# Optimization experiments

Hardware: AMD Instinct MI355X
Metric: run time of the kernel (lower is better)

Reference implementation:

```python
import jax, jax.numpy as jnp
import numpy as np

D = 2048          # input_dim == dec_hidden_size
S = 16384         # src_time_steps
H = 250           # projection hidden (hard-coded in module)


def setup_inputs() -> dict:
    key = jax.random.key(0)
    ks = jax.random.split(key, 12)
    sc_d = 1.0 / np.sqrt(D)
    sc_3d = 1.0 / np.sqrt(3 * D)
    sc_h = 1.0 / np.sqrt(H)
    return {
        "s_prev": jax.random.normal(ks[0], (1, 1, D), jnp.float32),
        "enc_hs": jax.random.normal(ks[1], (1, S, D), jnp.float32),
        "cur_men_rep": jax.random.normal(ks[2], (1, 1, D), jnp.float32),
        "src_mask": jax.random.randint(ks[3], (1, S), 0, 2, jnp.int32),
        "W_info": jax.random.normal(ks[4], (D, D), jnp.float32) * sc_d,
        "W_ctx": jax.random.normal(ks[5], (D, D), jnp.float32) * sc_d,
        "W_q": jax.random.normal(ks[6], (D, D), jnp.float32) * sc_d,
        "b_q": jnp.zeros((D,), jnp.float32),
        "W_p1": jax.random.normal(ks[7], (H, 3 * D), jnp.float32) * sc_3d,
        "b_p1": jnp.zeros((H,), jnp.float32),
        "W_p2": jax.random.normal(ks[8], (1, H), jnp.float32) * sc_h,
        "b_p2": jnp.zeros((1,), jnp.float32),
    }


def reference(s_prev, enc_hs, cur_men_rep, src_mask,
              W_info, W_ctx, W_q, b_q, W_p1, b_p1, W_p2, b_p2):
    # dh = linear_info(cur_men_rep): [1,1,D]; uh = linear_ctx(enc_hs): [1,S,D]
    dh = jnp.einsum('bqe,de->bqd', cur_men_rep, W_info)
    uh = jnp.einsum('bse,de->bsd', enc_hs, W_ctx)
    wq = jnp.einsum('bqe,de->bqd', s_prev, W_q) + b_q
    # cat(uh, wq.repeat, dh.repeat) -> tanh : [1,S,3D]
    wquh = jnp.tanh(jnp.concatenate(
        [uh, jnp.broadcast_to(wq, uh.shape), jnp.broadcast_to(dh, uh.shape)],
        axis=2))
    # projection: Linear(3D,250) -> Dropout(eval: identity) -> ReLU -> Linear(250,1)
    h = jax.nn.relu(jnp.einsum('bsk,hk->bsh', wquh, W_p1) + b_p1)
    scores = (jnp.einsum('bsh,oh->bso', h, W_p2) + b_p2).squeeze()   # [S] (B=1)
    scores = jnp.where(src_mask.squeeze().astype(bool), -jnp.inf, scores)
    attn = jax.nn.softmax(scores, axis=-1)                            # [S]
    ctx = jnp.sum(enc_hs * attn[None, :, None], axis=1)               # [1,D]
    return attn, ctx
```

## Files before the change

kernel.cpp:

```cpp
#include <hip/hip_runtime.h>
#include <hip/hip_bf16.h>
#include <stdint.h>

#define DD 2048
#define SS 16384
#define HH 250
#define GEMMB_GRID 264

typedef __attribute__((ext_vector_type(8))) short bf16x8;
typedef __attribute__((ext_vector_type(4))) float f32x4;

__device__ __forceinline__ unsigned short f2bf(float f){
  union { float f; uint32_t u; } v; v.f = f;
  uint32_t u = v.u;
  return (unsigned short)((u + 0x7fffu + ((u >> 16) & 1u)) >> 16);
}
__device__ __forceinline__ float bf2f(unsigned short h){
  union { uint32_t u; float f; } v; v.u = ((uint32_t)h) << 16; return v.f;
}
__device__ __forceinline__ float fast_tanh(float x){
  return 1.0f - 2.0f / (1.0f + __expf(2.0f * x));
}
__device__ __forceinline__ void gl_lds16(const void* g, void* l){
  __builtin_amdgcn_global_load_lds((const __attribute__((address_space(1))) void*)g,
                                   (__attribute__((address_space(3))) void*)l, 16, 0, 0);
}

__global__ __launch_bounds__(256) void mega_kernel(
    const float* __restrict__ W_ctx, unsigned short* __restrict__ wctxb,
    const float* __restrict__ W_p1, unsigned short* __restrict__ wp1ab,
    const float* __restrict__ s_prev, const float* __restrict__ cmr,
    const float* __restrict__ Wq, const float* __restrict__ bq,
    const float* __restrict__ Winfo,
    float* __restrict__ twq, float* __restrict__ tdh,
    const int* __restrict__ mask, int* __restrict__ idx, int* __restrict__ cpos,
    int* __restrict__ mcount,
    const float* __restrict__ enc, unsigned short* __restrict__ encb)
{
  const int b = blockIdx.x, t = threadIdx.x;
  if(b == 0){
    __shared__ int cnt[256];
    const int base = t * 64;
    int c = 0;
    for(int i = 0; i < 64; i++) c += (mask[base + i] == 0);
    cnt[t] = c;
    __syncthreads();
    for(int off = 1; off < 256; off <<= 1){
      int v = (t >= off) ? cnt[t - off] : 0;
      __syncthreads();
      cnt[t] += v;
      __syncthreads();
    }
    int p = cnt[t] - c;
    for(int i = 0; i < 64; i++){
      int fi = base + i;
      if(mask[fi] == 0){ idx[p] = fi; cpos[fi] = p; p++; }
      else cpos[fi] = -1;
    }
    if(t == 255){
      int tot = cnt[255];
      mcount[0] = tot;
      mcount[1] = (tot + 255) & ~255;
      mcount[2] = (tot + 63) & ~63;
    }
  } else if(b < 2049){
    #pragma unroll
    for(int r = 0; r < 8; r++){
      int j = (b - 1) * 8 + r;
      const float4* p = (const float4*)(enc + (size_t)j * DD + t * 8);
      float4 a = p[0], c = p[1];
      bf16x8 v;
      v[0]=(short)f2bf(a.x); v[1]=(short)f2bf(a.y); v[2]=(short)f2bf(a.z); v[3]=(short)f2bf(a.w);
      v[4]=(short)f2bf(c.x); v[5]=(short)f2bf(c.y); v[6]=(short)f2bf(c.z); v[7]=(short)f2bf(c.w);
      *(bf16x8*)(encb + (size_t)j * DD + t * 8) = v;
    }
  } else if(b < 2561){
    for(int i = (b - 2049) * 256 + t; i < (DD * DD) / 8; i += 512 * 256){
      const float4* p = (const float4*)(W_ctx + (size_t)i * 8);
      float4 a = p[0], c = p[1];
      bf16x8 v;
      v[0]=(short)f2bf(a.x); v[1]=(short)f2bf(a.y); v[2]=(short)f2bf(a.z); v[3]=(short)f2bf(a.w);
      v[4]=(short)f2bf(c.x); v[5]=(short)f2bf(c.y); v[6]=(short)f2bf(c.z); v[7]=(short)f2bf(c.w);
      *(bf16x8*)(wctxb + (size_t)i * 8) = v;
    }
  } else if(b < 2817){
    int g = (b - 2561) * 256 + t;
    int row = g >> 8, col = (g & 255) * 8;
    int rc = row < HH ? row : HH - 1;
    const float* s = W_p1 + (size_t)rc * (3 * DD) + col;
    bf16x8 v;
    #pragma unroll
    for(int j = 0; j < 8; j++) v[j] = (row < HH) ? (short)f2bf(s[j]) : (short)0;
    *(bf16x8*)(wp1ab + (size_t)g * 8) = v;
  } else {
    int vb = b - 2817;
    int wid = t >> 6, lane = t & 63;
    bool isq = vb < 512;
    int r = (isq ? vb : vb - 512) * 4 + wid;
    const float* M = (isq ? Wq : Winfo) + (size_t)r * DD;
    const float* x = isq ? s_prev : cmr;
    float s = 0.f;
    for(int i = lane; i < DD; i += 64) s += M[i] * x[i];
    #pragma unroll
    for(int o = 32; o; o >>= 1) s += __shfl_xor(s, o);
    if(lane == 0){
      if(isq) twq[r] = fast_tanh(s + bq[r]);
      else    tdh[r] = fast_tanh(s);
    }
  }
}

__device__ __forceinline__ void stageA_idx(const unsigned short* __restrict__ g,
                                           const int* r2, int kt, char* ldsbase,
                                           int wid, int lane)
{
  const int srow = lane >> 3;
  const int c = (lane & 7) ^ srow;
  #pragma unroll
  for(int i = 0; i < 2; i++){
    int r8 = (wid * 2 + i) * 8;
    gl_lds16(g + (size_t)r2[i] * DD + kt + c * 8, ldsbase + r8 * 128);
  }
}
__device__ __forceinline__ void stage_half(const unsigned short* __restrict__ g,
                                           int grow0, int kt, char* ldsbase,
                                           int wid, int lane)
{
  const int srow = lane >> 3;
  const int c = (lane & 7) ^ srow;
  #pragma unroll
  for(int i = 0; i < 2; i++){
    int r8 = (wid * 2 + i) * 8;
    gl_lds16(g + (size_t)(grow0 + r8 + srow) * DD + kt + c * 8,
             ldsbase + r8 * 128);
  }
}
#define RDF(base, lr, kc) (*(const bf16x8*)((base) + (lr) * 128 + (((kc) * 16) ^ (((lr) & 7) << 4))))

__global__ __launch_bounds__(512, 2) void gemmA_kernel(
    const unsigned short* __restrict__ A, const int* __restrict__ idx,
    const unsigned short* __restrict__ B, const int* __restrict__ mcount,
    unsigned short* __restrict__ Ct,
    const float* __restrict__ wp1, const float* __restrict__ bp1,
    const float* __restrict__ twq, const float* __restrict__ tdh,
    float* __restrict__ bias2)
{
  const int tid = threadIdx.x, lane = tid & 63, wid = tid >> 6;
  if(blockIdx.x >= 512){
    int h = (blockIdx.x - 512) * 8 + wid;
    if(h >= HH){ if(lane == 0 && h < 256) bias2[h] = 0.f; return; }
    const float* r1 = wp1 + (size_t)h * (3 * DD) + DD;
    const float* r2 = wp1 + (size_t)h * (3 * DD) + 2 * DD;
    float s = 0.f;
    for(int i = lane; i < DD; i += 64) s += r1[i] * twq[i] + r2[i] * tdh[i];
    #pragma unroll
    for(int o = 32; o; o >>= 1) s += __shfl_xor(s, o);
    if(lane == 0) bias2[h] = s + bp1[h];
    return;
  }
  __shared__ alignas(128) char lds[131072];
  const int wm = wid >> 2, wn = wid & 3;
  const int slot = blockIdx.x >> 3;
  const int mt = (blockIdx.x & 7) + ((slot >> 3) << 3);
  const int n0 = (slot & 7) * 256;
  const int MT = mcount[1] >> 8;
  if(mt >= MT) return;
  const int m0 = mt * 256;
  const int frow = lane & 15, kch = lane >> 4;

  int ra0[2], ra1[2];
  {
    const int tot = mcount[0];
    const int srow = lane >> 3;
    #pragma unroll
    for(int i = 0; i < 2; i++){
      int r0 = m0 + (wid * 2 + i) * 8 + srow;
      int r1 = r0 + 128;
      ra0[i] = idx[r0 < tot ? r0 : tot - 1];
      ra1[i] = idx[r1 < tot ? r1 : tot - 1];
    }
  }

  f32x4 acc[8][4] = {};

  stageA_idx(A, ra0, 0, lds,         wid, lane);
  stageA_idx(A, ra1, 0, lds + 16384, wid, lane);
  stage_half(B, n0,        0, lds + 32768,         wid, lane);
  stage_half(B, n0 + 128,  0, lds + 49152,         wid, lane);
  stage_half(B, n0,       64, lds + 65536 + 32768, wid, lane);
  stage_half(B, n0 + 128, 64, lds + 65536 + 49152, wid, lane);
  asm volatile("s_waitcnt vmcnt(4)" ::: "memory");
  __builtin_amdgcn_s_barrier();

  #pragma unroll 2
  for(int t = 0; t < 32; t++){
    const int d = t & 1;
    char* Ab = lds + d * 65536;
    char* Bb = Ab + 32768;
    char* An = lds + (d ^ 1) * 65536;
    bf16x8 bfr[4][2];
    #pragma unroll
    for(int q = 0; q < 4; q++){
      if(q == 0){
        #pragma unroll
        for(int nr = 0; nr < 4; nr++){
          int row = wn * 64 + nr * 16 + frow;
          #pragma unroll
          for(int ks = 0; ks < 2; ks++) bfr[nr][ks] = RDF(Bb, row, ks * 4 + kch);
        }
      }
      bf16x8 afr[2][2];
      #pragma unroll
      for(int mi = 0; mi < 2; mi++){
        int row = wm * 128 + (q * 2 + mi) * 16 + frow;
        #pragma unroll
        for(int ks = 0; ks < 2; ks++) afr[mi][ks] = RDF(Ab, row, ks * 4 + kch);
      }
      if(q == 0){
        if(t + 1 < 32){
          stageA_idx(A, ra0, (t + 1) * 64, An,         wid, lane);
          stageA_idx(A, ra1, (t + 1) * 64, An + 16384, wid, lane);
        }
      } else if(q == 1){
        if(t + 2 < 32) stage_half(B, n0,       (t + 2) * 64, Bb,         wid, lane);
      } else if(q == 2){
        if(t + 2 < 32) stage_half(B, n0 + 128, (t + 2) * 64, Bb + 16384, wid, lane);
      }
      __builtin_amdgcn_s_barrier();
      __builtin_amdgcn_sched_barrier(0);
      __builtin_amdgcn_s_setprio(1);
      #pragma unroll
      for(int mi = 0; mi < 2; mi++)
        #pragma unroll
        for(int nr = 0; nr < 4; nr++)
          #pragma unroll
          for(int ks = 0; ks < 2; ks++)
            acc[q * 2 + mi][nr] = __builtin_amdgcn_mfma_f32_16x16x32_bf16(
                afr[mi][ks], bfr[nr][ks], acc[q * 2 + mi][nr], 0, 0, 0);
      __builtin_amdgcn_s_setprio(0);
      __builtin_amdgcn_sched_barrier(0);
      if(q == 3){
        if(t < 30)       asm volatile("s_waitcnt vmcnt(4)" ::: "memory");
        else if(t == 30) asm volatile("s_waitcnt vmcnt(0)" ::: "memory");
      }
      __builtin_amdgcn_s_barrier();
    }
  }

  const int r0 = m0 + wm * 128 + (lane >> 4) * 4;
  const int c0 = n0 + wn * 64 + frow;
  #pragma unroll
  for(int mr = 0; mr < 8; mr++)
    #pragma unroll
    for(int nr = 0; nr < 4; nr++)
      #pragma unroll
      for(int r = 0; r < 4; r++)
        Ct[(size_t)(r0 + mr * 16 + r) * DD + c0 + nr * 16] = f2bf(fast_tanh(acc[mr][nr][r]));
}

__global__ __launch_bounds__(512, 4) void gemmB_kernel(
    const unsigned short* __restrict__ A, const unsigned short* __restrict__ B,
    const int* __restrict__ mcount, const float* __restrict__ bias2,
    const float* __restrict__ w2, const float* __restrict__ bp2,
    float* __restrict__ attnc, float* __restrict__ Tpart)
{
  __shared__ alignas(128) char lds[81920];
  __shared__ float sred[8][32];
  const int tid = threadIdx.x, lane = tid & 63, wid = tid >> 6;
  const int wm = wid >> 2, wn = wid & 3;
  const int m0 = blockIdx.x * 64;
  const int mc0 = mcount[0], mc2 = mcount[2];
  if(m0 >= mc2){ if(tid == 0) Tpart[blockIdx.x] = 0.f; return; }
  const int frow = lane & 15, kch = lane >> 4;
  const int srow = lane >> 3, sc = ((lane & 7) ^ srow) * 8;

  f32x4 acc[2][4] = {};

  gl_lds16(A + (size_t)(m0 + wid * 8 + srow) * DD + sc, lds + wid * 1024);
  #pragma unroll
  for(int i = 0; i < 4; i++){
    int l = wid + 8 * i;
    gl_lds16(B + (size_t)(l * 8 + srow) * DD + sc,      lds + 16384 + l * 1024);
    gl_lds16(B + (size_t)(l * 8 + srow) * DD + 64 + sc, lds + 49152 + l * 1024);
  }
  asm volatile("s_waitcnt vmcnt(4)" ::: "memory");
  __builtin_amdgcn_s_barrier();

  #pragma unroll 2
  for(int t = 0; t < 32; t++){
    const int d = t & 1;
    char* Ab = lds + d * 8192;
    char* An = lds + (d ^ 1) * 8192;
    char* Bb = lds + 16384 + d * 32768;
    bf16x8 bfr[4][2], afr[2];
    #pragma unroll
    for(int q = 0; q < 2; q++){
      if(q == 0){
        #pragma unroll
        for(int nr = 0; nr < 4; nr++){
          int row = wn * 64 + nr * 16 + frow;
          #pragma unroll
          for(int ks = 0; ks < 2; ks++) bfr[nr][ks] = RDF(Bb, row, ks * 4 + kch);
        }
      }
      {
        int row = wm * 32 + q * 16 + frow;
        #pragma unroll
        for(int ks = 0; ks < 2; ks++) afr[ks] = RDF(Ab, row, ks * 4 + kch);
      }
      if(q == 0){
        if(t + 1 < 32)
          gl_lds16(A + (size_t)(m0 + wid * 8 + srow) * DD + (t + 1) * 64 + sc, An + wid * 1024);
      } else {
        if(t + 2 < 32){
          #pragma unroll
          for(int i = 0; i < 4; i++){
            int l = wid + 8 * i;
            gl_lds16(B + (size_t)(l * 8 + srow) * DD + (t + 2) * 64 + sc, Bb + l * 1024);
          }
        }
      }
      __builtin_amdgcn_s_barrier();
      __builtin_amdgcn_sched_barrier(0);
      __builtin_amdgcn_s_setprio(1);
      #pragma unroll
      for(int nr = 0; nr < 4; nr++)
        #pragma unroll
        for(int ks = 0; ks < 2; ks++)
          acc[q][nr] = __builtin_amdgcn_mfma_f32_16x16x32_bf16(afr[ks], bfr[nr][ks], acc[q][nr], 0, 0, 0);
      __builtin_amdgcn_s_setprio(0);
      __builtin_amdgcn_sched_barrier(0);
      if(q == 1){
        if(t < 30)       asm volatile("s_waitcnt vmcnt(4)" ::: "memory");
        else if(t == 30) asm volatile("s_waitcnt vmcnt(0)" ::: "memory");
      }
      __builtin_amdgcn_s_barrier();
    }
  }

  float w2v[4], b2v[4];
  #pragma unroll
  for(int in = 0; in < 4; in++){
    int n = wn * 64 + in * 16 + frow;
    w2v[in] = (n < HH) ? w2[n] : 0.f;
    b2v[in] = bias2[n];
  }
  #pragma unroll
  for(int mi = 0; mi < 2; mi++){
    #pragma unroll
    for(int r = 0; r < 4; r++){
      float s = 0.f;
      #pragma unroll
      for(int in = 0; in < 4; in++){
        float h = acc[mi][in][r] + b2v[in];
        s += (h > 0.f ? h : 0.f) * w2v[in];
      }
      s += __shfl_xor(s, 1); s += __shfl_xor(s, 2);
      s += __shfl_xor(s, 4); s += __shfl_xor(s, 8);
      if(frow == 0) sred[wid][mi * 16 + (lane >> 4) * 4 + r] = s;
    }
  }
  __syncthreads();
  if(tid < 64){
    int wmr = tid >> 5, rr = tid & 31;
    float s = sred[wmr * 4][rr] + sred[wmr * 4 + 1][rr] + sred[wmr * 4 + 2][rr]
            + sred[wmr * 4 + 3][rr] + bp2[0];
    int j = m0 + tid;
    float e = (j < mc0) ? __expf(s) : 0.f;
    if(j < mc0) attnc[j] = e;
    #pragma unroll
    for(int o = 32; o; o >>= 1) e += __shfl_xor(e, o);
    if(tid == 0) Tpart[blockIdx.x] = e;
  }
}

__global__ __launch_bounds__(256) void normctx_kernel(
    const float* __restrict__ attnc, const int* __restrict__ cpos,
    const int* __restrict__ idx, const int* __restrict__ mcount,
    const float* __restrict__ Tpart, const unsigned short* __restrict__ encb,
    float* __restrict__ out, float* __restrict__ part)
{
  const int b = blockIdx.x, t = threadIdx.x;
  if(b < 64){
    __shared__ float sT;
    if(t == 0){
      float s = 0.f;
      for(int i = 0; i < GEMMB_GRID; i++) s += Tpart[i];
      sT = 1.0f / s;
    }
    __syncthreads();
    int i = b * 256 + t;
    int cp = cpos[i];
    out[i] = (cp >= 0) ? attnc[cp] * sT : 0.f;
  } else {
    const int bb = b - 64;
    const int mc0 = mcount[0];
    const int chunk = (mc0 + 255) >> 8;
    const int j0 = bb * chunk;
    const int j1 = min(j0 + chunk, mc0);
    float a[8] = {};
    for(int j = j0; j < j1; j++){
      float e = attnc[j];
      bf16x8 v = *(const bf16x8*)(encb + (size_t)idx[j] * DD + t * 8);
      #pragma unroll
      for(int k = 0; k < 8; k++) a[k] += e * bf2f((unsigned short)v[k]);
    }
    float* o = part + (size_t)bb * DD + t * 8;
    #pragma unroll
    for(int k = 0; k < 8; k++) o[k] = a[k];
  }
}

__global__ __launch_bounds__(256) void ctxr_kernel(
    const float* __restrict__ part, const float* __restrict__ Tpart,
    float* __restrict__ out)
{
  __shared__ float sT;
  if(threadIdx.x == 0){
    float s = 0.f;
    for(int i = 0; i < GEMMB_GRID; i++) s += Tpart[i];
    sT = 1.0f / s;
  }
  __syncthreads();
  const int dcol = blockIdx.x * 256 + threadIdx.x;
  float s = 0.f;
  for(int b = 0; b < 256; b++) s += part[(size_t)b * DD + dcol];
  out[dcol] = s * sT;
}

extern "C" void kernel_launch(void* const* d_in, const int* in_sizes, int n_in,
                              void* d_out, int out_size, void* d_ws, size_t ws_size,
                              hipStream_t stream)
{
  const float* s_prev = (const float*)d_in[0];
  const float* enc    = (const float*)d_in[1];
  const float* cmr    = (const float*)d_in[2];
  const int*   mask   = (const int*)d_in[3];
  const float* W_info = (const float*)d_in[4];
  const float* W_ctx  = (const float*)d_in[5];
  const float* W_q    = (const float*)d_in[6];
  const float* b_q    = (const float*)d_in[7];
  const float* W_p1   = (const float*)d_in[8];
  const float* b_p1   = (const float*)d_in[9];
  const float* W_p2   = (const float*)d_in[10];
  const float* b_p2   = (const float*)d_in[11];
  float* out = (float*)d_out;

  char* ws = (char*)d_ws;
  unsigned short* encb    = (unsigned short*)(ws);
  unsigned short* tanhbuf = (unsigned short*)(ws + 67108864);
  unsigned short* wctxb   = (unsigned short*)(ws + 134217728);
  unsigned short* wp1ab   = (unsigned short*)(ws + 142606336);
  int*   idx    = (int*)(ws + 143654912);
  int*   cpos   = (int*)(ws + 143720448);
  float* attnc  = (float*)(ws + 143785984);
  float* part   = (float*)(ws + 143851520);
  float* twq    = (float*)(ws + 145948672);
  float* tdh    = (float*)(ws + 145956864);
  float* bias2  = (float*)(ws + 145965056);
  int*   mcount = (int*)(ws + 145966080);
  float* Tpart  = (float*)(ws + 145966208);

  mega_kernel<<<3841, 256, 0, stream>>>(W_ctx, wctxb, W_p1, wp1ab,
                                        s_prev, cmr, W_q, b_q, W_info,
                                        twq, tdh, mask, idx, cpos, mcount,
                                        enc, encb);
  gemmA_kernel<<<544, 512, 0, stream>>>(encb, idx, wctxb, mcount, tanhbuf,
                                        W_p1, b_p1, twq, tdh, bias2);
  gemmB_kernel<<<GEMMB_GRID, 512, 0, stream>>>(tanhbuf, wp1ab, mcount, bias2,
                                               W_p2, b_p2, attnc, Tpart);
  normctx_kernel<<<320, 256, 0, stream>>>(attnc, cpos, idx, mcount, Tpart,
                                          encb, out, part);
  ctxr_kernel<<<8, 256, 0, stream>>>(part, Tpart, out + SS);
}
```

Before: 222.3 us.

## Split mask scan into ballot-based kernel and coalesce bf16 conversion loads

Moves the mask compaction out of block 0 of the conversion kernel into a separate single-block, 1024-thread kernel that uses wave ballots and popcount instead of a per-thread serial 64-element scan. The fp32-to-bf16 conversion of enc_hs, W_ctx and W_p1 is restructured so each thread handles strided float4 chunks with several loads in flight, giving fully coalesced accesses and fewer blocks. The aim is to remove the long serial tail of block 0 and raise memory throughput in the conversion pass. The cost is one extra kernel launch on the critical path, and the scan no longer overlaps with the conversion work.

```diff
diff --git a/kernel.cpp b/kernel.cpp
--- a/kernel.cpp
+++ b/kernel.cpp
@@ -8,6 +8,7 @@
 #define GEMMB_GRID 264
 
 typedef __attribute__((ext_vector_type(8))) short bf16x8;
+typedef __attribute__((ext_vector_type(4))) short bf16x4;
 typedef __attribute__((ext_vector_type(4))) float f32x4;
 
 __device__ __forceinline__ unsigned short f2bf(float f){
@@ -18,6 +19,11 @@
 __device__ __forceinline__ float bf2f(unsigned short h){
   union { uint32_t u; float f; } v; v.u = ((uint32_t)h) << 16; return v.f;
 }
+__device__ __forceinline__ bf16x4 pk4(float4 a){
+  bf16x4 v;
+  v[0]=(short)f2bf(a.x); v[1]=(short)f2bf(a.y); v[2]=(short)f2bf(a.z); v[3]=(short)f2bf(a.w);
+  return v;
+}
 __device__ __forceinline__ float fast_tanh(float x){
   return 1.0f - 2.0f / (1.0f + __expf(2.0f * x));
 }
@@ -26,74 +32,90 @@
                                    (__attribute__((address_space(3))) void*)l, 16, 0, 0);
 }
 
+__global__ __launch_bounds__(1024) void scan_kernel(const int* __restrict__ mask,
+                                                    int* __restrict__ idx,
+                                                    int* __restrict__ cpos,
+                                                    int* __restrict__ mcount)
+{
+  __shared__ int wsum[16];
+  const int t = threadIdx.x, lane = t & 63, w = t >> 6;
+  int running = 0;
+  for(int k = 0; k < 16; k++){
+    const int e = k * 1024 + t;
+    const int m = (mask[e] == 0);
+    unsigned long long bal = __ballot(m);
+    if(lane == 0) wsum[w] = __popcll(bal);
+    __syncthreads();
+    int wpre = 0;
+    for(int i = 0; i < w; i++) wpre += wsum[i];
+    int tot = wpre;
+    for(int i = w; i < 16; i++) tot += wsum[i];
+    const int lpre = __popcll(bal & ((1ull << lane) - 1ull));
+    const int pos = running + wpre + lpre;
+    if(m){ idx[pos] = e; cpos[e] = pos; } else cpos[e] = -1;
+    running += tot;
+    __syncthreads();
+  }
+  if(t == 0){
+    mcount[0] = running;
+    mcount[1] = (running + 255) & ~255;
+    mcount[2] = (running + 63) & ~63;
+  }
+}
+
 __global__ __launch_bounds__(256) void mega_kernel(
+    const float* __restrict__ enc, unsigned short* __restrict__ encb,
     const float* __restrict__ W_ctx, unsigned short* __restrict__ wctxb,
     const float* __restrict__ W_p1, unsigned short* __restrict__ wp1ab,
     const float* __restrict__ s_prev, const float* __restrict__ cmr,
     const float* __restrict__ Wq, const float* __restrict__ bq,
     const float* __restrict__ Winfo,
-    float* __restrict__ twq, float* __restrict__ tdh,
-    const int* __restrict__ mask, int* __restrict__ idx, int* __restrict__ cpos,
-    int* __restrict__ mcount,
-    const float* __restrict__ enc, unsigned short* __restrict__ encb)
+    float* __restrict__ twq, float* __restrict__ tdh)
 {
   const int b = blockIdx.x, t = threadIdx.x;
-  if(b == 0){
-    __shared__ int cnt[256];
-    const int base = t * 64;
-    int c = 0;
-    for(int i = 0; i < 64; i++) c += (mask[base + i] == 0);
-    cnt[t] = c;
-    __syncthreads();
-    for(int off = 1; off < 256; off <<= 1){
-      int v = (t >= off) ? cnt[t - off] : 0;
-      __syncthreads();
-      cnt[t] += v;
-      __syncthreads();
-    }
-    int p = cnt[t] - c;
-    for(int i = 0; i < 64; i++){
-      int fi = base + i;
-      if(mask[fi] == 0){ idx[p] = fi; cpos[fi] = p; p++; }
-      else cpos[fi] = -1;
-    }
-    if(t == 255){
-      int tot = cnt[255];
-      mcount[0] = tot;
-      mcount[1] = (tot + 255) & ~255;
-      mcount[2] = (tot + 63) & ~63;
-    }
-  } else if(b < 2049){
-    #pragma unroll
-    for(int r = 0; r < 8; r++){
-      int j = (b - 1) * 8 + r;
-      const float4* p = (const float4*)(enc + (size_t)j * DD + t * 8);
-      float4 a = p[0], c = p[1];
-      bf16x8 v;
-      v[0]=(short)f2bf(a.x); v[1]=(short)f2bf(a.y); v[2]=(short)f2bf(a.z); v[3]=(short)f2bf(a.w);
-      v[4]=(short)f2bf(c.x); v[5]=(short)f2bf(c.y); v[6]=(short)f2bf(c.z); v[7]=(short)f2bf(c.w);
-      *(bf16x8*)(encb + (size_t)j * DD + t * 8) = v;
-    }
-  } else if(b < 2561){
-    for(int i = (b - 2049) * 256 + t; i < (DD * DD) / 8; i += 512 * 256){
-      const float4* p = (const float4*)(W_ctx + (size_t)i * 8);
-      float4 a = p[0], c = p[1];
-      bf16x8 v;
-      v[0]=(short)f2bf(a.x); v[1]=(short)f2bf(a.y); v[2]=(short)f2bf(a.z); v[3]=(short)f2bf(a.w);
-      v[4]=(short)f2bf(c.x); v[5]=(short)f2bf(c.y); v[6]=(short)f2bf(c.z); v[7]=(short)f2bf(c.w);
-      *(bf16x8*)(wctxb + (size_t)i * 8) = v;
-    }
-  } else if(b < 2817){
-    int g = (b - 2561) * 256 + t;
-    int row = g >> 8, col = (g & 255) * 8;
-    int rc = row < HH ? row : HH - 1;
-    const float* s = W_p1 + (size_t)rc * (3 * DD) + col;
-    bf16x8 v;
-    #pragma unroll
-    for(int j = 0; j < 8; j++) v[j] = (row < HH) ? (short)f2bf(s[j]) : (short)0;
-    *(bf16x8*)(wp1ab + (size_t)g * 8) = v;
+  if(b < 2048){
+    const float4* in4 = (const float4*)enc;
+    bf16x4* out4 = (bf16x4*)encb;
+    const int gt = b * 256 + t;
+    const int S = 524288;
+    #pragma unroll
+    for(int k = 0; k < 4; k++){
+      int i0 = gt + (4 * k + 0) * S, i1 = gt + (4 * k + 1) * S;
+      int i2 = gt + (4 * k + 2) * S, i3 = gt + (4 * k + 3) * S;
+      float4 a = in4[i0], c = in4[i1], d = in4[i2], e = in4[i3];
+      out4[i0] = pk4(a); out4[i1] = pk4(c); out4[i2] = pk4(d); out4[i3] = pk4(e);
+    }
+  } else if(b < 2304){
+    const float4* in4 = (const float4*)W_ctx;
+    bf16x4* out4 = (bf16x4*)wctxb;
+    const int gt = (b - 2048) * 256 + t;
+    const int S = 65536;
+    #pragma unroll
+    for(int k = 0; k < 4; k++){
+      int i0 = gt + (4 * k + 0) * S, i1 = gt + (4 * k + 1) * S;
+      int i2 = gt + (4 * k + 2) * S, i3 = gt + (4 * k + 3) * S;
+      float4 a = in4[i0], c = in4[i1], d = in4[i2], e = in4[i3];
+      out4[i0] = pk4(a); out4[i1] = pk4(c); out4[i2] = pk4(d); out4[i3] = pk4(e);
+    }
+  } else if(b < 2336){
+    bf16x4* out4 = (bf16x4*)wp1ab;
+    const int gt = (b - 2304) * 256 + t;
+    const int S = 8192;
+    #pragma unroll
+    for(int k = 0; k < 16; k++){
+      int i = gt + k * S;
+      int row = i >> 9, col = i & 511;
+      bf16x4 v;
+      if(row < HH){
+        float4 a = *(const float4*)(W_p1 + (size_t)row * (3 * DD) + (col << 2));
+        v = pk4(a);
+      } else {
+        v[0] = 0; v[1] = 0; v[2] = 0; v[3] = 0;
+      }
+      out4[i] = v;
+    }
   } else {
-    int vb = b - 2817;
+    int vb = b - 2336;
     int wid = t >> 6, lane = t & 63;
     bool isq = vb < 512;
     int r = (isq ? vb : vb - 512) * 4 + wid;
@@ -461,10 +483,9 @@
   int*   mcount = (int*)(ws + 145966080);
   float* Tpart  = (float*)(ws + 145966208);
 
-  mega_kernel<<<3841, 256, 0, stream>>>(W_ctx, wctxb, W_p1, wp1ab,
-                                        s_prev, cmr, W_q, b_q, W_info,
-                                        twq, tdh, mask, idx, cpos, mcount,
-                                        enc, encb);
+  mega_kernel<<<3360, 256, 0, stream>>>(enc, encb, W_ctx, wctxb, W_p1, wp1ab,
+                                        s_prev, cmr, W_q, b_q, W_info, twq, tdh);
+  scan_kernel<<<1, 1024, 0, stream>>>(mask, idx, cpos, mcount);
   gemmA_kernel<<<544, 512, 0, stream>>>(encb, idx, wctxb, mcount, tanhbuf,
                                         W_p1, b_p1, twq, tdh, bias2);
   gemmB_kernel<<<GEMMB_GRID, 512, 0, stream>>>(tanhbuf, wp1ab, mcount, bias2,
```

New measurement: 216.8 us. 1.03x faster.
